# Kernel tuning notes

Measured on AMD Instinct MI355X. Metric: run time of the kernel, lower is better.

The kernel has to match this reference:

```python
import jax, jax.numpy as jnp
import numpy as np
import math

B, L, D, H, NT, T, NLAYERS = 64, 128, 512, 8, 10000, 65536, 2
DH = D // H
FF = 2 * D
EPS = 1e-5


def setup_inputs() -> dict:
    key = jax.random.key(0)
    ks = jax.random.split(key, 20)
    item_ids = jax.random.randint(ks[0], (T,), 0, NT, dtype=jnp.int32)
    seg_ids = jnp.sort(jax.random.randint(ks[1], (T,), 0, B * L, dtype=jnp.int32))
    pad_mask = jnp.zeros((B, L), dtype=bool)
    future_mask = jnp.where(jnp.triu(jnp.ones((L, L), dtype=bool), k=1), -1e9, 0.0).astype(jnp.float32)

    s = 0.02
    emb = (jax.random.normal(ks[2], (NT + 1, D), jnp.float32) * s).at[NT].set(0.0)  # padding_idx row is zero
    Wqkv = jax.random.normal(ks[3], (NLAYERS, 3 * D, D), jnp.float32) * s
    bqkv = jnp.zeros((NLAYERS, 3 * D), jnp.float32)
    Wo = jax.random.normal(ks[4], (NLAYERS, D, D), jnp.float32) * s
    bo = jnp.zeros((NLAYERS, D), jnp.float32)
    W1 = jax.random.normal(ks[5], (NLAYERS, FF, D), jnp.float32) * s
    b1 = jnp.zeros((NLAYERS, FF), jnp.float32)
    W2 = jax.random.normal(ks[6], (NLAYERS, D, FF), jnp.float32) * s
    b2 = jnp.zeros((NLAYERS, D), jnp.float32)
    ln1_s = jnp.ones((NLAYERS, D), jnp.float32)
    ln1_b = jnp.zeros((NLAYERS, D), jnp.float32)
    ln2_s = jnp.ones((NLAYERS, D), jnp.float32)
    ln2_b = jnp.zeros((NLAYERS, D), jnp.float32)
    Wout = jax.random.normal(ks[7], (NT, D), jnp.float32) * s
    bout = jnp.zeros((NT,), jnp.float32)
    return dict(item_ids=item_ids, seg_ids=seg_ids, pad_mask=pad_mask, future_mask=future_mask,
                max_len=L, emb=emb, Wqkv=Wqkv, bqkv=bqkv, Wo=Wo, bo=bo, W1=W1, b1=b1, W2=W2, b2=b2,
                ln1_s=ln1_s, ln1_b=ln1_b, ln2_s=ln2_s, ln2_b=ln2_b, Wout=Wout, bout=bout)


def _layernorm(x, s, b):
    m = jnp.mean(x, axis=-1, keepdims=True)
    v = jnp.mean(jnp.square(x - m), axis=-1, keepdims=True)
    return (x - m) * jax.lax.rsqrt(v + EPS) * s + b


def _pos_encoding(maxlen, d):
    den = jnp.exp(-jnp.arange(0, d, 2, dtype=jnp.float32) * (math.log(10000.0) / d))
    pos = jnp.arange(maxlen, dtype=jnp.float32)[:, None]
    pe = jnp.zeros((maxlen, d), jnp.float32)
    pe = pe.at[:, 0::2].set(jnp.sin(pos * den))
    pe = pe.at[:, 1::2].set(jnp.cos(pos * den))
    return pe


def reference(item_ids, seg_ids, pad_mask, future_mask, max_len, emb,
              Wqkv, bqkv, Wo, bo, W1, b1, W2, b2, ln1_s, ln1_b, ln2_s, ln2_b, Wout, bout):
    # fused gather + segment-mean (replaces the per-user Python loops)
    counts = jax.ops.segment_sum(jnp.ones((T,), jnp.float32), seg_ids, num_segments=B * max_len)
    sums = jax.ops.segment_sum(emb[item_ids], seg_ids, num_segments=B * max_len)  # [B*L, D]
    means = jnp.where(counts[:, None] > 0, sums / jnp.maximum(counts, 1.0)[:, None], 0.0)
    x = means.reshape(B, max_len, D) + _pos_encoding(max_len, D)

    key_mask = jnp.where(pad_mask[:, None, None, :], -1e9, 0.0)  # [B,1,1,L]
    scale = 1.0 / math.sqrt(DH)
    for i in range(NLAYERS):
        qkv = x @ Wqkv[i].T + bqkv[i]                         # [B,L,3D]
        q, k, v = jnp.split(qkv, 3, axis=-1)
        q = q.reshape(B, max_len, H, DH)
        k = k.reshape(B, max_len, H, DH)
        v = v.reshape(B, max_len, H, DH)
        scores = jnp.einsum('bqhd,bkhd->bhqk', q, k) * scale + future_mask + key_mask
        attn = jax.nn.softmax(scores, axis=-1)
        o = jnp.einsum('bhqk,bkhd->bqhd', attn, v).reshape(B, max_len, D)
        o = o @ Wo[i].T + bo[i]
        x = _layernorm(x + o, ln1_s[i], ln1_b[i])              # post-norm
        ff = jax.nn.relu(x @ W1[i].T + b1[i]) @ W2[i].T + b2[i]
        x = _layernorm(x + ff, ln2_s[i], ln2_b[i])
    return x @ Wout.T + bout  # [B, L, num_types]
```

## Files before the change

### kernel.cpp

```cpp
#include <hip/hip_runtime.h>

#define T_TOTAL 65536
#define SEQ 128
#define DMODEL 512
#define DHEAD 64
#define NTYPES 10000
#define ROWS 8192
#define NOUT_PAD 10240

typedef float floatx4 __attribute__((ext_vector_type(4)));
typedef short shortx8 __attribute__((ext_vector_type(8)));

#define GLOAD_LDS(gp, lp) __builtin_amdgcn_global_load_lds( \
    (const __attribute__((address_space(1))) void*)(gp),    \
    (__attribute__((address_space(3))) void*)(lp), 16, 0, 0)

#define MFMA_BF16 __builtin_amdgcn_mfma_f32_16x16x32_bf16

__device__ __forceinline__ unsigned short f2bf(float f) {
  union { float f; unsigned u; } v; v.f = f;
  unsigned u = v.u + 0x7fffu + ((v.u >> 16) & 1u);
  return (unsigned short)(u >> 16);
}

__device__ __forceinline__ void phase_barrier() {
  __builtin_amdgcn_sched_barrier(0);
  __builtin_amdgcn_s_barrier();
  __builtin_amdgcn_sched_barrier(0);
}

__global__ __launch_bounds__(256) void convert_pad_kernel(
    const float* __restrict__ src, unsigned short* __restrict__ dst,
    long nsrc, long ndst) {
  long i = (long)blockIdx.x * 1024 + (long)threadIdx.x * 4;
  if (i >= ndst) return;
  float4 v = make_float4(0.f, 0.f, 0.f, 0.f);
  if (i < nsrc) v = *(const float4*)(src + i);
  ushort4 o;
  o.x = f2bf(v.x); o.y = f2bf(v.y); o.z = f2bf(v.z); o.w = f2bf(v.w);
  *(ushort4*)(dst + i) = o;
}

__global__ __launch_bounds__(128) void seg_mean_kernel(
    const int* __restrict__ item_ids, const int* __restrict__ seg_ids,
    const float* __restrict__ emb, float* __restrict__ x_f,
    unsigned short* __restrict__ x_b) {
  int s = blockIdx.x;
  int lo = 0, hi = T_TOTAL;
  while (lo < hi) { int mid = (lo + hi) >> 1; if (seg_ids[mid] < s) lo = mid + 1; else hi = mid; }
  int start = lo;
  hi = T_TOTAL;
  while (lo < hi) { int mid = (lo + hi) >> 1; if (seg_ids[mid] <= s) lo = mid + 1; else hi = mid; }
  int end = lo;
  int c = threadIdx.x << 2;
  float4 acc = make_float4(0.f, 0.f, 0.f, 0.f);
  for (int j = start; j < end; ++j) {
    const float* e = emb + (long)item_ids[j] * DMODEL + c;
    float4 v = *(const float4*)e;
    acc.x += v.x; acc.y += v.y; acc.z += v.z; acc.w += v.w;
  }
  int cnt = end - start;
  float inv = cnt > 0 ? 1.0f / (float)cnt : 0.0f;
  float mv[4] = {acc.x * inv, acc.y * inv, acc.z * inv, acc.w * inv};
  int l = s & (SEQ - 1);
  const float klog = 0.017988946039015984f;
  long base = (long)s * DMODEL + c;
#pragma unroll
  for (int t = 0; t < 4; ++t) {
    int col = c + t;
    float den = expf(-(float)(col & ~1) * klog);
    float ang = (float)l * den;
    float pe = (col & 1) ? cosf(ang) : sinf(ang);
    float val = mv[t] + pe;
    x_f[base + t] = val;
    x_b[base + t] = f2bf(val);
  }
}

__global__ __launch_bounds__(256) void gemm_bt_kernel(
    const unsigned short* __restrict__ A,
    const unsigned short* __restrict__ B,
    const float* __restrict__ bias,
    float* __restrict__ Cf,
    unsigned short* __restrict__ Cb,
    int K, int Nreal, int ldC, int relu) {
  __shared__ unsigned short As[128 * 32];
  __shared__ unsigned short Bs[128 * 32];
  const int tid = threadIdx.x;
  const int lane = tid & 63;
  const int wave = tid >> 6;
  const int wm = (wave >> 1) << 6;
  const int wn = (wave & 1) << 6;
  const int l16 = lane & 15;
  const int quad = lane >> 4;
  const long rowA0 = (long)blockIdx.x * 128;
  const long rowB0 = (long)blockIdx.y * 128;

  floatx4 acc[4][4] = {};

  const int rowOff = tid >> 2;
  const int kOff = (tid & 3) << 3;
  const unsigned short* gA = A + (rowA0 + rowOff) * (long)K + kOff;
  const unsigned short* gB = B + (rowB0 + rowOff) * (long)K + kOff;
  unsigned short* lA = As + tid * 8;
  unsigned short* lB = Bs + tid * 8;

  for (int k0 = 0; k0 < K; k0 += 32) {
    __syncthreads();
    GLOAD_LDS(gA + k0, lA);
    GLOAD_LDS(gA + 64 * (long)K + k0, lA + 2048);
    GLOAD_LDS(gB + k0, lB);
    GLOAD_LDS(gB + 64 * (long)K + k0, lB + 2048);
    __syncthreads();
    shortx8 af[4], bfr[4];
#pragma unroll
    for (int i = 0; i < 4; ++i)
      af[i] = *(const shortx8*)(As + (wm + i * 16 + l16) * 32 + quad * 8);
#pragma unroll
    for (int j = 0; j < 4; ++j)
      bfr[j] = *(const shortx8*)(Bs + (wn + j * 16 + l16) * 32 + quad * 8);
#pragma unroll
    for (int i = 0; i < 4; ++i)
#pragma unroll
      for (int j = 0; j < 4; ++j)
        acc[i][j] = MFMA_BF16(af[i], bfr[j], acc[i][j], 0, 0, 0);
  }

#pragma unroll
  for (int i = 0; i < 4; ++i) {
    int row = (int)rowA0 + wm + i * 16 + quad * 4;
#pragma unroll
    for (int j = 0; j < 4; ++j) {
      int col = (int)rowB0 + wn + j * 16 + l16;
      if (col < Nreal) {
        float bv = bias ? bias[col] : 0.0f;
#pragma unroll
        for (int r = 0; r < 4; ++r) {
          float v = acc[i][j][r] + bv;
          if (relu) v = fmaxf(v, 0.0f);
          long off = (long)(row + r) * ldC + col;
          if (Cf) Cf[off] = v;
          if (Cb) Cb[off] = f2bf(v);
        }
      }
    }
  }
}

__global__ __launch_bounds__(512, 2) void gemm256_kernel(
    const unsigned short* __restrict__ A,
    const unsigned short* __restrict__ B,
    const float* __restrict__ bias,
    float* __restrict__ Cf,
    unsigned short* __restrict__ Cb,
    int K, int Nreal, int ldC, int relu) {
  __shared__ unsigned short As[2][256 * 64];
  __shared__ unsigned short Bs[2][256 * 64];
  const int tid = threadIdx.x;
  const int lane = tid & 63;
  const int wave = tid >> 6;
  const int wm = wave >> 2;
  const int wn = wave & 3;
  const int l16 = lane & 15;
  const int quad = lane >> 4;
  const long rowA0 = (long)blockIdx.x * 256;
  const long rowB0 = (long)blockIdx.y * 256;

  floatx4 acc[8][4] = {};

  const int srow = tid >> 3;
  const int scol = (tid & 7) << 3;
  const unsigned short* gA = A + (rowA0 + srow) * (long)K + scol;
  const unsigned short* gB = B + (rowB0 + srow) * (long)K + scol;
  const int loff = tid * 8;
  const long rstep = 64 * (long)K;

#pragma unroll
  for (int is = 0; is < 4; ++is) {
    GLOAD_LDS(gA + is * rstep, &As[0][is * 4096 + loff]);
    GLOAD_LDS(gB + is * rstep, &Bs[0][is * 4096 + loff]);
  }
  asm volatile("s_waitcnt vmcnt(0)" ::: "memory");
  phase_barrier();

  const int KT = K >> 6;
  for (int kt = 0; kt < KT; ++kt) {
    const int cur = kt & 1;
    const unsigned short* Ab = As[cur];
    const unsigned short* Bb = Bs[cur];
    unsigned short* An = As[cur ^ 1];
    unsigned short* Bn = Bs[cur ^ 1];
    const bool stage = (kt + 1) < KT;
    const unsigned short* gAn = gA + (long)(kt + 1) * 64;
    const unsigned short* gBn = gB + (long)(kt + 1) * 64;

    shortx8 af[4][2], bf[4][2];

#pragma unroll
    for (int m = 0; m < 4; ++m) {
      const unsigned short* p = Ab + (wm * 128 + m * 16 + l16) * 64 + quad * 8;
      af[m][0] = *(const shortx8*)(p);
      af[m][1] = *(const shortx8*)(p + 32);
    }
#pragma unroll
    for (int n = 0; n < 2; ++n) {
      const unsigned short* p = Bb + (wn * 64 + n * 16 + l16) * 64 + quad * 8;
      bf[n][0] = *(const shortx8*)(p);
      bf[n][1] = *(const shortx8*)(p + 32);
    }
    if (stage) {
      GLOAD_LDS(gAn, An + loff);
      GLOAD_LDS(gAn + rstep, An + 4096 + loff);
    }
    phase_barrier();
    __builtin_amdgcn_s_setprio(1);
#pragma unroll
    for (int m = 0; m < 4; ++m)
#pragma unroll
      for (int n = 0; n < 2; ++n) {
        acc[m][n] = MFMA_BF16(af[m][0], bf[n][0], acc[m][n], 0, 0, 0);
        acc[m][n] = MFMA_BF16(af[m][1], bf[n][1], acc[m][n], 0, 0, 0);
      }
    __builtin_amdgcn_s_setprio(0);
    phase_barrier();

#pragma unroll
    for (int n = 2; n < 4; ++n) {
      const unsigned short* p = Bb + (wn * 64 + n * 16 + l16) * 64 + quad * 8;
      bf[n][0] = *(const shortx8*)(p);
      bf[n][1] = *(const shortx8*)(p + 32);
    }
    if (stage) {
      GLOAD_LDS(gAn + 2 * rstep, An + 8192 + loff);
      GLOAD_LDS(gAn + 3 * rstep, An + 12288 + loff);
    }
    phase_barrier();
    __builtin_amdgcn_s_setprio(1);
#pragma unroll
    for (int m = 0; m < 4; ++m)
#pragma unroll
      for (int n = 2; n < 4; ++n) {
        acc[m][n] = MFMA_BF16(af[m][0], bf[n][0], acc[m][n], 0, 0, 0);
        acc[m][n] = MFMA_BF16(af[m][1], bf[n][1], acc[m][n], 0, 0, 0);
      }
    __builtin_amdgcn_s_setprio(0);
    phase_barrier();

#pragma unroll
    for (int m = 0; m < 4; ++m) {
      const unsigned short* p = Ab + (wm * 128 + 64 + m * 16 + l16) * 64 + quad * 8;
      af[m][0] = *(const shortx8*)(p);
      af[m][1] = *(const shortx8*)(p + 32);
    }
    if (stage) {
      GLOAD_LDS(gBn, Bn + loff);
      GLOAD_LDS(gBn + rstep, Bn + 4096 + loff);
    }
    phase_barrier();
    __builtin_amdgcn_s_setprio(1);
#pragma unroll
    for (int m = 0; m < 4; ++m)
#pragma unroll
      for (int n = 0; n < 2; ++n) {
        acc[4 + m][n] = MFMA_BF16(af[m][0], bf[n][0], acc[4 + m][n], 0, 0, 0);
        acc[4 + m][n] = MFMA_BF16(af[m][1], bf[n][1], acc[4 + m][n], 0, 0, 0);
      }
    __builtin_amdgcn_s_setprio(0);
    phase_barrier();

    if (stage) {
      GLOAD_LDS(gBn + 2 * rstep, Bn + 8192 + loff);
      GLOAD_LDS(gBn + 3 * rstep, Bn + 12288 + loff);
    }
    phase_barrier();
    __builtin_amdgcn_s_setprio(1);
#pragma unroll
    for (int m = 0; m < 4; ++m)
#pragma unroll
      for (int n = 2; n < 4; ++n) {
        acc[4 + m][n] = MFMA_BF16(af[m][0], bf[n][0], acc[4 + m][n], 0, 0, 0);
        acc[4 + m][n] = MFMA_BF16(af[m][1], bf[n][1], acc[4 + m][n], 0, 0, 0);
      }
    __builtin_amdgcn_s_setprio(0);
    asm volatile("s_waitcnt vmcnt(0)" ::: "memory");
    phase_barrier();
  }

#pragma unroll
  for (int m = 0; m < 8; ++m) {
    int row = (int)rowA0 + wm * 128 + m * 16 + quad * 4;
#pragma unroll
    for (int n = 0; n < 4; ++n) {
      int col = (int)rowB0 + wn * 64 + n * 16 + l16;
      if (col < Nreal) {
        float bv = bias ? bias[col] : 0.0f;
#pragma unroll
        for (int r = 0; r < 4; ++r) {
          float v = acc[m][n][r] + bv;
          if (relu) v = fmaxf(v, 0.0f);
          long off = (long)(row + r) * ldC + col;
          if (Cf) Cf[off] = v;
          if (Cb) Cb[off] = f2bf(v);
        }
      }
    }
  }
}

__global__ __launch_bounds__(256) void attn_kernel(
    const float* __restrict__ qkv,
    unsigned short* __restrict__ o_b) {
  __shared__ float Ks[SEQ * DHEAD];
  __shared__ float Vs[SEQ * DHEAD];
  __shared__ float Ds[SEQ];
  int b = blockIdx.x >> 3, h = blockIdx.x & 7;
  const float* base = qkv + (long)b * SEQ * 1536;
  int hoff = h * DHEAD;
  for (int idx = threadIdx.x; idx < SEQ * DHEAD; idx += 256) {
    int l = idx >> 6, c = idx & 63;
    Ks[idx] = base[l * 1536 + 512 + hoff + c];
    Vs[idx] = base[l * 1536 + 1024 + hoff + c];
  }
  __syncthreads();
  int l = threadIdx.x & 127;
  int half = threadIdx.x >> 7;
  float q[DHEAD];
#pragma unroll
  for (int c = 0; c < DHEAD; ++c) q[c] = base[l * 1536 + hoff + c];
  float o[DHEAD];
#pragma unroll
  for (int c = 0; c < DHEAD; ++c) o[c] = 0.f;
  float denom = 0.f;
  for (int j = half; j <= l; j += 2) {
    const float* kr = Ks + j * DHEAD;
    float s0 = 0.f, s1 = 0.f, s2 = 0.f, s3 = 0.f;
#pragma unroll
    for (int c = 0; c < DHEAD; c += 4) {
      s0 += q[c] * kr[c];         s1 += q[c + 1] * kr[c + 1];
      s2 += q[c + 2] * kr[c + 2]; s3 += q[c + 3] * kr[c + 3];
    }
    float p = __expf(((s0 + s1) + (s2 + s3)) * 0.125f);
    denom += p;
    const float* vr = Vs + j * DHEAD;
#pragma unroll
    for (int c = 0; c < DHEAD; ++c) o[c] += p * vr[c];
  }
  __syncthreads();
  if (half) {
    float* os = Ks + l * DHEAD;
#pragma unroll
    for (int c = 0; c < DHEAD; ++c) os[c] = o[c];
    Ds[l] = denom;
  }
  __syncthreads();
  if (!half) {
    float dtot = denom + Ds[l];
    float inv = 1.0f / dtot;
    const float* os = Ks + l * DHEAD;
    unsigned short* dst = o_b + ((long)b * SEQ + l) * DMODEL + hoff;
#pragma unroll
    for (int c = 0; c < DHEAD; ++c) dst[c] = f2bf((o[c] + os[c]) * inv);
  }
}

__global__ __launch_bounds__(256) void add_ln_kernel(
    const float* __restrict__ x_in, const float* __restrict__ delta,
    const float* __restrict__ gamma, const float* __restrict__ beta,
    float* __restrict__ x_f, unsigned short* __restrict__ x_b) {
  int row = blockIdx.x;
  int tid = threadIdx.x;
  long base = (long)row * DMODEL;
  int c = tid * 2;
  float2 xv = *(const float2*)(x_in + base + c);
  float2 dv = *(const float2*)(delta + base + c);
  float a = xv.x + dv.x, b = xv.y + dv.y;
  float s = a + b;
  float sq = a * a + b * b;
#pragma unroll
  for (int off = 32; off > 0; off >>= 1) {
    s += __shfl_down(s, off, 64);
    sq += __shfl_down(sq, off, 64);
  }
  __shared__ float red[8];
  __shared__ float mean_s, rstd_s;
  int wv = tid >> 6, ln = tid & 63;
  if (ln == 0) { red[wv] = s; red[4 + wv] = sq; }
  __syncthreads();
  if (tid == 0) {
    float S = red[0] + red[1] + red[2] + red[3];
    float SQ = red[4] + red[5] + red[6] + red[7];
    float mean = S * (1.0f / 512.0f);
    float var = SQ * (1.0f / 512.0f) - mean * mean;
    mean_s = mean;
    rstd_s = rsqrtf(var + 1e-5f);
  }
  __syncthreads();
  float mean = mean_s, rstd = rstd_s;
  float o0 = (a - mean) * rstd * gamma[c] + beta[c];
  float o1 = (b - mean) * rstd * gamma[c + 1] + beta[c + 1];
  x_f[base + c] = o0;
  x_f[base + c + 1] = o1;
  x_b[base + c] = f2bf(o0);
  x_b[base + c + 1] = f2bf(o1);
}

extern "C" void kernel_launch(void* const* d_in, const int* in_sizes, int n_in,
                              void* d_out, int out_size, void* d_ws, size_t ws_size,
                              hipStream_t stream) {
  const int* item_ids = (const int*)d_in[0];
  const int* seg_ids = (const int*)d_in[1];
  const float* emb  = (const float*)d_in[5];
  const float* Wqkv = (const float*)d_in[6];
  const float* bqkv = (const float*)d_in[7];
  const float* Wo   = (const float*)d_in[8];
  const float* bo   = (const float*)d_in[9];
  const float* W1   = (const float*)d_in[10];
  const float* b1   = (const float*)d_in[11];
  const float* W2   = (const float*)d_in[12];
  const float* b2   = (const float*)d_in[13];
  const float* ln1s = (const float*)d_in[14];
  const float* ln1b = (const float*)d_in[15];
  const float* ln2s = (const float*)d_in[16];
  const float* ln2b = (const float*)d_in[17];
  const float* Wout = (const float*)d_in[18];
  const float* bout = (const float*)d_in[19];
  float* out = (float*)d_out;

  char* ws = (char*)d_ws;
  size_t off = 0;
  auto alloc = [&](size_t bytes) {
    void* p = ws + off;
    off += (bytes + 255) & ~(size_t)255;
    return p;
  };
  float* x_f  = (float*)alloc((size_t)ROWS * 512 * 4);
  unsigned short* x_b = (unsigned short*)alloc((size_t)ROWS * 512 * 2);
  float* qkv_f = (float*)alloc((size_t)ROWS * 1536 * 4);
  unsigned short* o_b = (unsigned short*)alloc((size_t)ROWS * 512 * 2);
  float* tmp_f = (float*)alloc((size_t)ROWS * 512 * 4);
  unsigned short* h_b = (unsigned short*)alloc((size_t)ROWS * 1024 * 2);
  unsigned short* wqkv_b = (unsigned short*)alloc((size_t)2 * 1536 * 512 * 2);
  unsigned short* wo_b = (unsigned short*)alloc((size_t)2 * 512 * 512 * 2);
  unsigned short* w1_b = (unsigned short*)alloc((size_t)2 * 1024 * 512 * 2);
  unsigned short* w2_b = (unsigned short*)alloc((size_t)2 * 512 * 1024 * 2);
  unsigned short* wout_b = (unsigned short*)alloc((size_t)NOUT_PAD * 512 * 2);

  auto cvt = [&](const float* src, unsigned short* dst, long nsrc, long ndst) {
    unsigned blocks = (unsigned)((ndst + 1023) / 1024);
    convert_pad_kernel<<<blocks, 256, 0, stream>>>(src, dst, nsrc, ndst);
  };
  cvt(Wqkv, wqkv_b, 2L * 1536 * 512, 2L * 1536 * 512);
  cvt(Wo, wo_b, 2L * 512 * 512, 2L * 512 * 512);
  cvt(W1, w1_b, 2L * 1024 * 512, 2L * 1024 * 512);
  cvt(W2, w2_b, 2L * 512 * 1024, 2L * 512 * 1024);
  cvt(Wout, wout_b, (long)NTYPES * 512, (long)NOUT_PAD * 512);

  seg_mean_kernel<<<ROWS, 128, 0, stream>>>(item_ids, seg_ids, emb, x_f, x_b);

  for (int i = 0; i < 2; ++i) {
    gemm256_kernel<<<dim3(32, 6), 512, 0, stream>>>(
        x_b, wqkv_b + (long)i * 1536 * 512, bqkv + i * 1536,
        qkv_f, nullptr, 512, 1536, 1536, 0);
    attn_kernel<<<512, 256, 0, stream>>>(qkv_f, o_b);
    gemm_bt_kernel<<<dim3(64, 4), 256, 0, stream>>>(
        o_b, wo_b + (long)i * 512 * 512, bo + i * 512,
        tmp_f, nullptr, 512, 512, 512, 0);
    add_ln_kernel<<<ROWS, 256, 0, stream>>>(x_f, tmp_f, ln1s + i * 512, ln1b + i * 512, x_f, x_b);
    gemm_bt_kernel<<<dim3(64, 8), 256, 0, stream>>>(
        x_b, w1_b + (long)i * 1024 * 512, b1 + i * 1024,
        nullptr, h_b, 512, 1024, 1024, 1);
    gemm_bt_kernel<<<dim3(64, 4), 256, 0, stream>>>(
        h_b, w2_b + (long)i * 512 * 1024, b2 + i * 512,
        tmp_f, nullptr, 1024, 512, 512, 0);
    add_ln_kernel<<<ROWS, 256, 0, stream>>>(x_f, tmp_f, ln2s + i * 512, ln2b + i * 512, x_f, x_b);
  }

  gemm256_kernel<<<dim3(32, 40), 512, 0, stream>>>(
      x_b, wout_b, bout, out, nullptr, 512, NTYPES, NTYPES, 0);
}
```

Baseline: 941.9 us.

## Swizzle GEMM LDS layout, batch weight conversion, vectorize attention loads and stores

The five per-tensor weight conversion launches become one grid-stride kernel. gemm256 stores its LDS tiles with an XOR swizzle on the 16-byte chunk index, so fragment reads avoid bank conflicts. It also regroups the global-to-LDS prefetch: all A tiles are issued in the first phase, all B tiles in the second, and one barrier phase is dropped. The attention kernel now uses float4 loads for Q, K and V and writes its bf16 output as 16-byte vectors. Together these aim to cut launch overhead, LDS bank conflicts and scalar memory traffic, at the cost of a burstier prefetch schedule.

```diff
diff --git a/kernel.cpp b/kernel.cpp
--- a/kernel.cpp
+++ b/kernel.cpp
@@ -29,16 +29,33 @@
   __builtin_amdgcn_sched_barrier(0);
 }
 
-__global__ __launch_bounds__(256) void convert_pad_kernel(
-    const float* __restrict__ src, unsigned short* __restrict__ dst,
-    long nsrc, long ndst) {
-  long i = (long)blockIdx.x * 1024 + (long)threadIdx.x * 4;
-  if (i >= ndst) return;
-  float4 v = make_float4(0.f, 0.f, 0.f, 0.f);
-  if (i < nsrc) v = *(const float4*)(src + i);
-  ushort4 o;
-  o.x = f2bf(v.x); o.y = f2bf(v.y); o.z = f2bf(v.z); o.w = f2bf(v.w);
-  *(ushort4*)(dst + i) = o;
+__global__ __launch_bounds__(256) void convert_all_kernel(
+    const float* __restrict__ Wqkv, const float* __restrict__ Wo,
+    const float* __restrict__ W1, const float* __restrict__ W2,
+    const float* __restrict__ Wout,
+    unsigned short* __restrict__ wqkv_b, unsigned short* __restrict__ wo_b,
+    unsigned short* __restrict__ w1_b, unsigned short* __restrict__ w2_b,
+    unsigned short* __restrict__ wout_b) {
+  const long Q0 = 1572864L / 4;
+  const long Q1 = Q0 + 524288L / 4;
+  const long Q2 = Q1 + 1048576L / 4;
+  const long Q3 = Q2 + 1048576L / 4;
+  const long Q4 = Q3 + 5242880L / 4;
+  const long stride = 2048L * 256;
+  for (long q = (long)blockIdx.x * 256 + threadIdx.x; q < Q4; q += stride) {
+    const float* src; unsigned short* dst; long i; bool guard = false;
+    if (q < Q0)      { src = Wqkv; dst = wqkv_b; i = q; }
+    else if (q < Q1) { src = Wo;   dst = wo_b;   i = q - Q0; }
+    else if (q < Q2) { src = W1;   dst = w1_b;   i = q - Q1; }
+    else if (q < Q3) { src = W2;   dst = w2_b;   i = q - Q2; }
+    else             { src = Wout; dst = wout_b; i = q - Q3; guard = true; }
+    long e = i * 4;
+    float4 v = make_float4(0.f, 0.f, 0.f, 0.f);
+    if (!guard || e < 5120000L) v = *(const float4*)(src + e);
+    ushort4 o;
+    o.x = f2bf(v.x); o.y = f2bf(v.y); o.z = f2bf(v.z); o.w = f2bf(v.w);
+    *(ushort4*)(dst + e) = o;
+  }
 }
 
 __global__ __launch_bounds__(128) void seg_mean_kernel(
@@ -147,6 +164,14 @@
   }
 }
 
+__device__ __forceinline__ void frag_read(const unsigned short* __restrict__ base,
+                                          int R, int quad, shortx8& f0, shortx8& f1) {
+  int pc = quad ^ (R & 7);
+  const unsigned short* p = base + R * 64;
+  f0 = *(const shortx8*)(p + pc * 8);
+  f1 = *(const shortx8*)(p + (pc ^ 4) * 8);
+}
+
 __global__ __launch_bounds__(512, 2) void gemm256_kernel(
     const unsigned short* __restrict__ A,
     const unsigned short* __restrict__ B,
@@ -169,7 +194,7 @@
   floatx4 acc[8][4] = {};
 
   const int srow = tid >> 3;
-  const int scol = (tid & 7) << 3;
+  const int scol = (((tid & 7) ^ ((tid >> 3) & 7)) << 3);
   const unsigned short* gA = A + (rowA0 + srow) * (long)K + scol;
   const unsigned short* gB = B + (rowB0 + srow) * (long)K + scol;
   const int loff = tid * 8;
@@ -197,20 +222,16 @@
     shortx8 af[4][2], bf[4][2];
 
 #pragma unroll
-    for (int m = 0; m < 4; ++m) {
-      const unsigned short* p = Ab + (wm * 128 + m * 16 + l16) * 64 + quad * 8;
-      af[m][0] = *(const shortx8*)(p);
-      af[m][1] = *(const shortx8*)(p + 32);
-    }
-#pragma unroll
-    for (int n = 0; n < 2; ++n) {
-      const unsigned short* p = Bb + (wn * 64 + n * 16 + l16) * 64 + quad * 8;
-      bf[n][0] = *(const shortx8*)(p);
-      bf[n][1] = *(const shortx8*)(p + 32);
-    }
+    for (int m = 0; m < 4; ++m)
+      frag_read(Ab, wm * 128 + m * 16 + l16, quad, af[m][0], af[m][1]);
+#pragma unroll
+    for (int n = 0; n < 2; ++n)
+      frag_read(Bb, wn * 64 + n * 16 + l16, quad, bf[n][0], bf[n][1]);
     if (stage) {
       GLOAD_LDS(gAn, An + loff);
       GLOAD_LDS(gAn + rstep, An + 4096 + loff);
+      GLOAD_LDS(gAn + 2 * rstep, An + 8192 + loff);
+      GLOAD_LDS(gAn + 3 * rstep, An + 12288 + loff);
     }
     phase_barrier();
     __builtin_amdgcn_s_setprio(1);
@@ -225,14 +246,13 @@
     phase_barrier();
 
 #pragma unroll
-    for (int n = 2; n < 4; ++n) {
-      const unsigned short* p = Bb + (wn * 64 + n * 16 + l16) * 64 + quad * 8;
-      bf[n][0] = *(const shortx8*)(p);
-      bf[n][1] = *(const shortx8*)(p + 32);
-    }
+    for (int n = 2; n < 4; ++n)
+      frag_read(Bb, wn * 64 + n * 16 + l16, quad, bf[n][0], bf[n][1]);
     if (stage) {
-      GLOAD_LDS(gAn + 2 * rstep, An + 8192 + loff);
-      GLOAD_LDS(gAn + 3 * rstep, An + 12288 + loff);
+      GLOAD_LDS(gBn, Bn + loff);
+      GLOAD_LDS(gBn + rstep, Bn + 4096 + loff);
+      GLOAD_LDS(gBn + 2 * rstep, Bn + 8192 + loff);
+      GLOAD_LDS(gBn + 3 * rstep, Bn + 12288 + loff);
     }
     phase_barrier();
     __builtin_amdgcn_s_setprio(1);
@@ -247,15 +267,8 @@
     phase_barrier();
 
 #pragma unroll
-    for (int m = 0; m < 4; ++m) {
-      const unsigned short* p = Ab + (wm * 128 + 64 + m * 16 + l16) * 64 + quad * 8;
-      af[m][0] = *(const shortx8*)(p);
-      af[m][1] = *(const shortx8*)(p + 32);
-    }
-    if (stage) {
-      GLOAD_LDS(gBn, Bn + loff);
-      GLOAD_LDS(gBn + rstep, Bn + 4096 + loff);
-    }
+    for (int m = 0; m < 4; ++m)
+      frag_read(Ab, wm * 128 + 64 + m * 16 + l16, quad, af[m][0], af[m][1]);
     phase_barrier();
     __builtin_amdgcn_s_setprio(1);
 #pragma unroll
@@ -268,11 +281,6 @@
     __builtin_amdgcn_s_setprio(0);
     phase_barrier();
 
-    if (stage) {
-      GLOAD_LDS(gBn + 2 * rstep, Bn + 8192 + loff);
-      GLOAD_LDS(gBn + 3 * rstep, Bn + 12288 + loff);
-    }
-    phase_barrier();
     __builtin_amdgcn_s_setprio(1);
 #pragma unroll
     for (int m = 0; m < 4; ++m)
@@ -316,17 +324,19 @@
   int b = blockIdx.x >> 3, h = blockIdx.x & 7;
   const float* base = qkv + (long)b * SEQ * 1536;
   int hoff = h * DHEAD;
-  for (int idx = threadIdx.x; idx < SEQ * DHEAD; idx += 256) {
-    int l = idx >> 6, c = idx & 63;
-    Ks[idx] = base[l * 1536 + 512 + hoff + c];
-    Vs[idx] = base[l * 1536 + 1024 + hoff + c];
+  for (int idx4 = threadIdx.x; idx4 < SEQ * DHEAD / 4; idx4 += 256) {
+    int l = idx4 >> 4;
+    int c4 = (idx4 & 15) << 2;
+    *(float4*)(Ks + l * 64 + c4) = *(const float4*)(base + l * 1536 + 512 + hoff + c4);
+    *(float4*)(Vs + l * 64 + c4) = *(const float4*)(base + l * 1536 + 1024 + hoff + c4);
   }
   __syncthreads();
   int l = threadIdx.x & 127;
   int half = threadIdx.x >> 7;
   float q[DHEAD];
 #pragma unroll
-  for (int c = 0; c < DHEAD; ++c) q[c] = base[l * 1536 + hoff + c];
+  for (int c4 = 0; c4 < 16; ++c4)
+    *(float4*)(q + c4 * 4) = *(const float4*)(base + l * 1536 + hoff + c4 * 4);
   float o[DHEAD];
 #pragma unroll
   for (int c = 0; c < DHEAD; ++c) o[c] = 0.f;
@@ -359,7 +369,13 @@
     const float* os = Ks + l * DHEAD;
     unsigned short* dst = o_b + ((long)b * SEQ + l) * DMODEL + hoff;
 #pragma unroll
-    for (int c = 0; c < DHEAD; ++c) dst[c] = f2bf((o[c] + os[c]) * inv);
+    for (int c0 = 0; c0 < DHEAD; c0 += 8) {
+      shortx8 ov;
+#pragma unroll
+      for (int k = 0; k < 8; ++k)
+        ov[k] = (short)f2bf((o[c0 + k] + os[c0 + k]) * inv);
+      *(shortx8*)(dst + c0) = ov;
+    }
   }
 }
 
@@ -445,15 +461,8 @@
   unsigned short* w2_b = (unsigned short*)alloc((size_t)2 * 512 * 1024 * 2);
   unsigned short* wout_b = (unsigned short*)alloc((size_t)NOUT_PAD * 512 * 2);
 
-  auto cvt = [&](const float* src, unsigned short* dst, long nsrc, long ndst) {
-    unsigned blocks = (unsigned)((ndst + 1023) / 1024);
-    convert_pad_kernel<<<blocks, 256, 0, stream>>>(src, dst, nsrc, ndst);
-  };
-  cvt(Wqkv, wqkv_b, 2L * 1536 * 512, 2L * 1536 * 512);
-  cvt(Wo, wo_b, 2L * 512 * 512, 2L * 512 * 512);
-  cvt(W1, w1_b, 2L * 1024 * 512, 2L * 1024 * 512);
-  cvt(W2, w2_b, 2L * 512 * 1024, 2L * 512 * 1024);
-  cvt(Wout, wout_b, (long)NTYPES * 512, (long)NOUT_PAD * 512);
+  convert_all_kernel<<<2048, 256, 0, stream>>>(
+      Wqkv, Wo, W1, W2, Wout, wqkv_b, wo_b, w1_b, w2_b, wout_b);
 
   seg_mean_kernel<<<ROWS, 128, 0, stream>>>(item_ids, seg_ids, emb, x_f, x_b);
 
```

Measured after the change: 899.4 us. 4.5% less time.
